# Optimization experiments

Hardware: AMD Instinct MI355X
Metric: run time of the kernel (lower is better)

Reference implementation:

```python
import jax, jax.numpy as jnp
import numpy as np

B, N, NKV = 2, 2048, 2048
E = 4096
H = 16
HD = E // H          # 256 head_dim
LQ = E // 8          # 512 q latent
LKV = E // 16        # 256 kv latent


def setup_inputs() -> dict:
    key = jax.random.key(0)
    ks = jax.random.split(key, 6)
    Q = jax.random.normal(ks[0], (B, N, E), dtype=jnp.float32)
    K = jax.random.normal(ks[1], (B, NKV, E), dtype=jnp.float32)
    # Linear weights stored as (in, out); scaled ~1/sqrt(fan_in) like torch default init
    Wq_d = jax.random.normal(ks[2], (E, LQ), dtype=jnp.float32) / np.sqrt(E)
    W_qk = jax.random.normal(ks[3], (LQ, H * LKV), dtype=jnp.float32) / np.sqrt(LQ)
    Wkv_d = jax.random.normal(ks[4], (E, LKV), dtype=jnp.float32) / np.sqrt(E)
    Wv_u = jax.random.normal(ks[5], (LKV, H * HD), dtype=jnp.float32) / np.sqrt(LKV)
    return {"Q": Q, "K": K, "Wq_d": Wq_d, "W_qk": W_qk, "Wkv_d": Wkv_d, "Wv_u": Wv_u}


def reference(Q, K, Wq_d, W_qk, Wkv_d, Wv_u):
    b, n, _ = Q.shape
    nkv = K.shape[1]
    C_q = Q @ Wq_d                                   # [B,N,Lq]
    C_kv = K @ Wkv_d                                 # [B,Nkv,Lkv]
    CqWqk = (C_q @ W_qk).reshape(b, n, H, LKV)       # [B,N,H,Lkv]
    # scores contract over the kv latent dim (absorbed-weight MLA)
    scores = jnp.einsum('bnhl,bkl->bhnk', CqWqk, C_kv) / jnp.sqrt(
        jnp.asarray(LKV, dtype=Q.dtype))             # [B,H,N,Nkv]
    attn = jax.nn.softmax(scores, axis=-1)
    V_up = (C_kv @ Wv_u).reshape(b, nkv, H, HD)      # [B,Nkv,H,hd]
    out = jnp.einsum('bhnk,bkhd->bnhd', attn, V_up)  # [B,N,H,hd]
    return out.reshape(b, n, H * HD)                 # [B,N,E]
```

## Files before the change

kernel.cpp:

```cpp
#include <hip/hip_runtime.h>


#define B_ 2
#define N_ 2048
#define H_ 16
#define HD_ 256
#define LKV_ 256

typedef __attribute__((ext_vector_type(8))) short bf8;
typedef __attribute__((ext_vector_type(4))) float f4;
typedef __attribute__((ext_vector_type(4))) unsigned short us4v;
typedef unsigned short u16;

__device__ __forceinline__ u16 f2b(float f) {
  union { float f; unsigned u; } v; v.f = f;
  unsigned r = (v.u + 0x7FFFu + ((v.u >> 16) & 1u)) >> 16;
  return (u16)r;
}

__device__ __forceinline__ void load_lds16(const void* g, void* l) {
  __builtin_amdgcn_global_load_lds(
      (const __attribute__((address_space(1))) unsigned int*)(unsigned long long)(uintptr_t)g,
      (__attribute__((address_space(3))) unsigned int*)(unsigned int)(uintptr_t)l,
      16, 0, 0);
}

__global__ __launch_bounds__(256) void cvt_bf16_2(const float* __restrict__ a,
                                                  u16* __restrict__ da,
                                                  const float* __restrict__ b,
                                                  u16* __restrict__ db, int n4)
{
  int i = blockIdx.x * 256 + threadIdx.x;
  const float* s; u16* d;
  if (i < n4) { s = a; d = da; } else { s = b; d = db; i -= n4; }
  float4 v = *(const float4*)(s + (size_t)i * 4);
  us4v o = {f2b(v.x), f2b(v.y), f2b(v.z), f2b(v.w)};
  *(us4v*)(d + (size_t)i * 4) = o;
}

__global__ __launch_bounds__(256) void cvt_transpose(const float* __restrict__ src,
                                                     u16* __restrict__ dst, int R, int C)
{
  __shared__ float tile[32][33];
  const int t = threadIdx.x;
  const int tr = t & 31, tc = t >> 5;
  const int r0 = blockIdx.x * 32, c0 = blockIdx.y * 32;
#pragma unroll
  for (int i = 0; i < 4; ++i)
    tile[tc + i * 8][tr] = src[(size_t)(r0 + tc + i * 8) * C + c0 + tr];
  __syncthreads();
#pragma unroll
  for (int i = 0; i < 4; ++i)
    dst[(size_t)(c0 + tc + i * 8) * R + r0 + tr] = f2b(tile[tr][tc + i * 8]);
}

__global__ __launch_bounds__(256) void gemm_bt(
    const u16* __restrict__ A,
    const u16* __restrict__ Bt,
    u16* __restrict__ C,
    int M, int N, int K)
{
  __shared__ u16 As[128 * 32];
  __shared__ u16 Bs[128 * 32];

  const int t = threadIdx.x;
  const int w = t >> 6, lane = t & 63;
  const int quad = lane >> 4, l16 = lane & 15;
  const int n0 = blockIdx.x * 128, m0 = blockIdx.y * 128;
  const int wm = (w >> 1) * 64, wn = (w & 1) * 64;

  f4 acc[4][4];
#pragma unroll
  for (int mi = 0; mi < 4; ++mi)
#pragma unroll
    for (int ni = 0; ni < 4; ++ni) acc[mi][ni] = (f4){0.f, 0.f, 0.f, 0.f};

  const u16* Ap = A + (size_t)m0 * K;
  const u16* Bp = Bt + (size_t)n0 * K;
  const int srow = t >> 2, spos = (t & 3) * 8;

  for (int k0 = 0; k0 < K; k0 += 32) {
    __syncthreads();
    load_lds16(Ap + (size_t)srow * K + k0 + spos,        &As[(size_t)t * 8]);
    load_lds16(Ap + (size_t)(srow + 64) * K + k0 + spos, &As[(size_t)(256 + t) * 8]);
    load_lds16(Bp + (size_t)srow * K + k0 + spos,        &Bs[(size_t)t * 8]);
    load_lds16(Bp + (size_t)(srow + 64) * K + k0 + spos, &Bs[(size_t)(256 + t) * 8]);
    __syncthreads();

    bf8 af[4], bfr[4];
#pragma unroll
    for (int mi = 0; mi < 4; ++mi)
      af[mi] = *(const bf8*)(&As[(wm + mi * 16 + l16) * 32 + quad * 8]);
#pragma unroll
    for (int ni = 0; ni < 4; ++ni)
      bfr[ni] = *(const bf8*)(&Bs[(wn + ni * 16 + l16) * 32 + quad * 8]);
#pragma unroll
    for (int mi = 0; mi < 4; ++mi)
#pragma unroll
      for (int ni = 0; ni < 4; ++ni)
        acc[mi][ni] = __builtin_amdgcn_mfma_f32_16x16x32_bf16(af[mi], bfr[ni], acc[mi][ni], 0, 0, 0);
  }

  u16* Cp = C + (size_t)m0 * N + n0;
#pragma unroll
  for (int mi = 0; mi < 4; ++mi)
#pragma unroll
    for (int r = 0; r < 4; ++r) {
      int m = wm + mi * 16 + quad * 4 + r;
#pragma unroll
      for (int ni = 0; ni < 4; ++ni)
        Cp[(size_t)m * N + wn + ni * 16 + l16] = f2b(acc[mi][ni][r]);
    }
}

__global__ __launch_bounds__(256) void gemm_qkv(
    const u16* __restrict__ Aq, const u16* __restrict__ Bq, u16* __restrict__ Cq,
    const u16* __restrict__ Ak, const u16* __restrict__ Bk, u16* __restrict__ Ck)
{
  const int K = 4096;
  __shared__ u16 As[128 * 32];
  __shared__ u16 Bs[64 * 32];

  const u16* A; const u16* Bt; u16* C; int N, n0;
  if (blockIdx.x < 8) { A = Aq; Bt = Bq; C = Cq; N = 512; n0 = blockIdx.x * 64; }
  else               { A = Ak; Bt = Bk; C = Ck; N = 256; n0 = (blockIdx.x - 8) * 64; }

  const int t = threadIdx.x;
  const int w = t >> 6, lane = t & 63;
  const int quad = lane >> 4, l16 = lane & 15;
  const int m0 = blockIdx.y * 128;
  const int wm = (w >> 1) * 64, wn = (w & 1) * 32;

  f4 acc[4][2];
#pragma unroll
  for (int mi = 0; mi < 4; ++mi)
#pragma unroll
    for (int ni = 0; ni < 2; ++ni) acc[mi][ni] = (f4){0.f, 0.f, 0.f, 0.f};

  const u16* Ap = A + (size_t)m0 * K;
  const u16* Bp = Bt + (size_t)n0 * K;
  const int srow = t >> 2, spos = (t & 3) * 8;

  for (int k0 = 0; k0 < K; k0 += 32) {
    __syncthreads();
    load_lds16(Ap + (size_t)srow * K + k0 + spos,        &As[(size_t)t * 8]);
    load_lds16(Ap + (size_t)(srow + 64) * K + k0 + spos, &As[(size_t)(256 + t) * 8]);
    load_lds16(Bp + (size_t)srow * K + k0 + spos,        &Bs[(size_t)t * 8]);
    __syncthreads();

    bf8 af[4], bfr[2];
#pragma unroll
    for (int mi = 0; mi < 4; ++mi)
      af[mi] = *(const bf8*)(&As[(wm + mi * 16 + l16) * 32 + quad * 8]);
#pragma unroll
    for (int ni = 0; ni < 2; ++ni)
      bfr[ni] = *(const bf8*)(&Bs[(wn + ni * 16 + l16) * 32 + quad * 8]);
#pragma unroll
    for (int mi = 0; mi < 4; ++mi)
#pragma unroll
      for (int ni = 0; ni < 2; ++ni)
        acc[mi][ni] = __builtin_amdgcn_mfma_f32_16x16x32_bf16(af[mi], bfr[ni], acc[mi][ni], 0, 0, 0);
  }

  u16* Cp = C + (size_t)m0 * N + n0;
#pragma unroll
  for (int mi = 0; mi < 4; ++mi)
#pragma unroll
    for (int r = 0; r < 4; ++r) {
      int m = wm + mi * 16 + quad * 4 + r;
#pragma unroll
      for (int ni = 0; ni < 2; ++ni)
        Cp[(size_t)m * N + wn + ni * 16 + l16] = f2b(acc[mi][ni][r]);
    }
}

__global__ __launch_bounds__(256) void transpose_v(const u16* __restrict__ vupB,
                                                   u16* __restrict__ vupT)
{
  __shared__ u16 tile[64][78];
  const int t = threadIdx.x;
  const int key0 = blockIdx.x * 64, d0 = blockIdx.y * 64;
  const int bh = blockIdx.z, b = bh >> 4, h = bh & 15;

#pragma unroll
  for (int i = 0; i < 2; ++i) {
    int c = t + 256 * i;
    int key = c >> 3, d8 = c & 7;
    bf8 v = *(const bf8*)(vupB + ((size_t)(b * N_ + key0 + key) * (H_ * HD_)) + h * HD_ + d0 + d8 * 8);
    *(bf8*)(&tile[key][d8 * 8]) = v;
  }
  __syncthreads();
#pragma unroll
  for (int i = 0; i < 2; ++i) {
    int c = t + 256 * i;
    int d = c >> 3, k8 = c & 7;
    bf8 v;
#pragma unroll
    for (int j = 0; j < 8; ++j) v[j] = (short)tile[k8 * 8 + j][d];
    *(bf8*)(vupT + ((size_t)bh * HD_ + d0 + d) * (size_t)N_ + key0 + k8 * 8) = v;
  }
}

__global__ __launch_bounds__(256, 3) void flash_mfma(
    const u16* __restrict__ q2b,
    const u16* __restrict__ ckvb,
    const u16* __restrict__ vupT,
    float* __restrict__ out)
{
  __shared__ u16 KtL[32 * 256];
  __shared__ u16 VtL[256 * 32];
  __shared__ u16 PtL[64 * 36];

  const int t = threadIdx.x;
  const int w = t >> 6, lane = t & 63;
  const int quad = lane >> 4, l16 = lane & 15;

  const int wg = blockIdx.x;
  const int xcd = wg & 7, idx = wg >> 3;
  const int bh = xcd * 4 + (idx >> 5);
  const int n0 = (idx & 31) * 64;
  const int b = bh >> 4, h = bh & 15;

  bf8 qf[8];
  {
    const u16* qbase = q2b + (size_t)(b * N_ + n0 + w * 16 + l16) * (H_ * LKV_) + h * LKV_ + quad * 8;
#pragma unroll
    for (int ks = 0; ks < 8; ++ks)
      qf[ks] = *(const bf8*)(qbase + ks * 32);
  }

  f4 o[16];
#pragma unroll
  for (int dt = 0; dt < 16; ++dt) o[dt] = (f4){0.f, 0.f, 0.f, 0.f};
  float ms[4], ls[4];
#pragma unroll
  for (int r = 0; r < 4; ++r) { ms[r] = -1e30f; ls[r] = 0.f; }

  const u16* kgb = ckvb + (size_t)b * N_ * LKV_;
  const u16* vgb = vupT + (size_t)bh * HD_ * N_;

  const int kswz = l16 & 7;
  const int vq8  = (quad ^ (l16 & 3)) * 8;

  for (int k0 = 0; k0 < N_; k0 += 32) {
    __syncthreads();
#pragma unroll
    for (int i = 0; i < 4; ++i) {
      int c = i * 256 + t;
      int kr = c >> 5, kc = (c & 31) ^ (kr & 7);
      load_lds16(kgb + (size_t)(k0 + kr) * LKV_ + kc * 8, &KtL[c * 8]);
    }
#pragma unroll
    for (int i = 0; i < 4; ++i) {
      int c = i * 256 + t;
      int vr = c >> 2, vc = (c & 3) ^ (vr & 3);
      load_lds16(vgb + (size_t)vr * N_ + k0 + vc * 8, &VtL[c * 8]);
    }
    __syncthreads();

    f4 sf[2];
    sf[0] = (f4){0,0,0,0}; sf[1] = (f4){0,0,0,0};
    __builtin_amdgcn_s_setprio(1);
#pragma unroll
    for (int nt = 0; nt < 2; ++nt) {
      const u16* kr = &KtL[(nt * 16 + l16) * 256];
#pragma unroll
      for (int ks = 0; ks < 8; ++ks) {
        bf8 kf = *(const bf8*)(kr + (((quad + ks * 4) ^ kswz) << 3));
        sf[nt] = __builtin_amdgcn_mfma_f32_16x16x32_bf16(qf[ks], kf, sf[nt], 0, 0, 0);
      }
    }
    __builtin_amdgcn_s_setprio(0);

    float al[4];
#pragma unroll
    for (int r = 0; r < 4; ++r) {
      float a0 = sf[0][r] * 0.0625f;
      float a1 = sf[1][r] * 0.0625f;
      float mx = fmaxf(a0, a1);
#pragma unroll
      for (int off = 1; off < 16; off <<= 1) mx = fmaxf(mx, __shfl_xor(mx, off, 16));
      float mn = fmaxf(ms[r], mx);
      float p0 = __expf(a0 - mn), p1 = __expf(a1 - mn);
      float sum = p0 + p1;
#pragma unroll
      for (int off = 1; off < 16; off <<= 1) sum += __shfl_xor(sum, off, 16);
      al[r] = __expf(ms[r] - mn);
      ls[r] = ls[r] * al[r] + sum;
      ms[r] = mn;
      int q = w * 16 + quad * 4 + r;
      PtL[q * 36 + l16]      = f2b(p0);
      PtL[q * 36 + 16 + l16] = f2b(p1);
    }
#pragma unroll
    for (int dt = 0; dt < 16; ++dt) {
      o[dt][0] *= al[0]; o[dt][1] *= al[1];
      o[dt][2] *= al[2]; o[dt][3] *= al[3];
    }

    bf8 pf = *(const bf8*)(&PtL[(w * 16 + l16) * 36 + quad * 8]);

    __builtin_amdgcn_s_setprio(1);
#pragma unroll
    for (int dt = 0; dt < 16; ++dt) {
      bf8 vf = *(const bf8*)(&VtL[(dt * 16 + l16) * 32 + vq8]);
      o[dt] = __builtin_amdgcn_mfma_f32_16x16x32_bf16(pf, vf, o[dt], 0, 0, 0);
    }
    __builtin_amdgcn_s_setprio(0);
  }

#pragma unroll
  for (int r = 0; r < 4; ++r) {
    float iv = 1.f / ls[r];
    float* dst = out + (size_t)(b * N_ + n0 + w * 16 + quad * 4 + r) * (H_ * HD_)
                 + h * HD_ + l16;
#pragma unroll
    for (int dt = 0; dt < 16; ++dt) dst[dt * 16] = o[dt][r] * iv;
  }
}

extern "C" void kernel_launch(void* const* d_in, const int* in_sizes, int n_in,
                              void* d_out, int out_size, void* d_ws, size_t ws_size,
                              hipStream_t stream) {
  const float* Q     = (const float*)d_in[0];
  const float* Kin   = (const float*)d_in[1];
  const float* Wq_d  = (const float*)d_in[2];
  const float* W_qk  = (const float*)d_in[3];
  const float* Wkv_d = (const float*)d_in[4];
  const float* Wv_u  = (const float*)d_in[5];
  float* out = (float*)d_out;

  char* ws = (char*)d_ws;
  u16* qbf   = (u16*)(ws);
  u16* vupT  = qbf;
  u16* kbf   = (u16*)(ws + 33554432);
  u16* vupB  = kbf;
  u16* q2b   = (u16*)(ws + 67108864);
  u16* cqb   = (u16*)(ws + 100663296);
  u16* ckvb  = (u16*)(ws + 104857600);
  u16* wqdT  = (u16*)(ws + 106954752);
  u16* wqkT  = (u16*)(ws + 111149056);
  u16* wkvdT = (u16*)(ws + 115343360);
  u16* wvuT  = (u16*)(ws + 117440512);

  cvt_bf16_2<<<dim3(32768), 256, 0, stream>>>(Q, qbf, Kin, kbf, 4194304);
  cvt_transpose<<<dim3(128, 16), 256, 0, stream>>>(Wq_d,  wqdT,  4096, 512);
  cvt_transpose<<<dim3(16, 128), 256, 0, stream>>>(W_qk,  wqkT,  512, 4096);
  cvt_transpose<<<dim3(128, 8),  256, 0, stream>>>(Wkv_d, wkvdT, 4096, 256);
  cvt_transpose<<<dim3(8, 128),  256, 0, stream>>>(Wv_u,  wvuT,  256, 4096);

  gemm_qkv<<<dim3(12, 32), 256, 0, stream>>>(qbf, wqdT, cqb, kbf, wkvdT, ckvb);
  gemm_bt<<<dim3(32, 32), 256, 0, stream>>>(cqb, wqkT, q2b, 4096, 4096, 512);
  gemm_bt<<<dim3(32, 32), 256, 0, stream>>>(ckvb, wvuT, vupB, 4096, 4096, 256);
  transpose_v<<<dim3(32, 4, 32), 256, 0, stream>>>(vupB, vupT);
  flash_mfma<<<dim3(1024), 256, 0, stream>>>(q2b, ckvb, vupT, out);
}
```

Baseline: 656.7 us.

## Give each flash-attention wave two query tiles and fold softmax scale into weights

The flash kernel now runs 2 waves of 128 threads per block, and each wave handles 32 query rows as two 16-row MFMA tiles. Every K and V fragment read from LDS is therefore reused for two MFMAs. The score MFMA operands are swapped so the row max and sum reductions take only two cross-quad shuffles. Row rescale factors and the final normalisers now pass through a small LDS array. The 1/16 softmax scale is folded into the bf16 conversion of W_qk, which removes the per-element multiply. In exchange, register pressure roughly doubles (o[2][16], qf[2][8]), each thread issues twice as many async loads, and per-block parallelism is halved.

```diff
diff --git a/kernel.cpp b/kernel.cpp
--- a/kernel.cpp
+++ b/kernel.cpp
@@ -39,7 +39,8 @@
 }
 
 __global__ __launch_bounds__(256) void cvt_transpose(const float* __restrict__ src,
-                                                     u16* __restrict__ dst, int R, int C)
+                                                     u16* __restrict__ dst, int R, int C,
+                                                     float scale)
 {
   __shared__ float tile[32][33];
   const int t = threadIdx.x;
@@ -51,7 +52,7 @@
   __syncthreads();
 #pragma unroll
   for (int i = 0; i < 4; ++i)
-    dst[(size_t)(c0 + tc + i * 8) * R + r0 + tr] = f2b(tile[tr][tc + i * 8]);
+    dst[(size_t)(c0 + tc + i * 8) * R + r0 + tr] = f2b(tile[tr][tc + i * 8] * scale);
 }
 
 __global__ __launch_bounds__(256) void gemm_bt(
@@ -201,7 +202,7 @@
   }
 }
 
-__global__ __launch_bounds__(256, 3) void flash_mfma(
+__global__ __launch_bounds__(128, 2) void flash_mfma(
     const u16* __restrict__ q2b,
     const u16* __restrict__ ckvb,
     const u16* __restrict__ vupT,
@@ -209,7 +210,8 @@
 {
   __shared__ u16 KtL[32 * 256];
   __shared__ u16 VtL[256 * 32];
-  __shared__ u16 PtL[64 * 36];
+  __shared__ u16 PtL[64 * 40];
+  __shared__ float alL[64];
 
   const int t = threadIdx.x;
   const int w = t >> 6, lane = t & 63;
@@ -221,45 +223,48 @@
   const int n0 = (idx & 31) * 64;
   const int b = bh >> 4, h = bh & 15;
 
-  bf8 qf[8];
+  bf8 qf[2][8];
   {
-    const u16* qbase = q2b + (size_t)(b * N_ + n0 + w * 16 + l16) * (H_ * LKV_) + h * LKV_ + quad * 8;
-#pragma unroll
-    for (int ks = 0; ks < 8; ++ks)
-      qf[ks] = *(const bf8*)(qbase + ks * 32);
-  }
-
-  f4 o[16];
-#pragma unroll
-  for (int dt = 0; dt < 16; ++dt) o[dt] = (f4){0.f, 0.f, 0.f, 0.f};
-  float ms[4], ls[4];
-#pragma unroll
-  for (int r = 0; r < 4; ++r) { ms[r] = -1e30f; ls[r] = 0.f; }
+    const u16* qbase = q2b + (size_t)(b * N_ + n0 + w * 32 + l16) * (H_ * LKV_) + h * LKV_ + quad * 8;
+#pragma unroll
+    for (int mi = 0; mi < 2; ++mi)
+#pragma unroll
+      for (int ks = 0; ks < 8; ++ks)
+        qf[mi][ks] = *(const bf8*)(qbase + (size_t)(mi * 16) * (H_ * LKV_) + ks * 32);
+  }
+
+  f4 o[2][16];
+#pragma unroll
+  for (int mi = 0; mi < 2; ++mi)
+#pragma unroll
+    for (int dt = 0; dt < 16; ++dt) o[mi][dt] = (f4){0.f, 0.f, 0.f, 0.f};
+  float ms[2] = {-1e30f, -1e30f}, ls[2] = {0.f, 0.f};
 
   const u16* kgb = ckvb + (size_t)b * N_ * LKV_;
   const u16* vgb = vupT + (size_t)bh * HD_ * N_;
 
   const int kswz = l16 & 7;
-  const int vq8  = (quad ^ (l16 & 3)) * 8;
+  const int vsl8 = (quad ^ ((l16 >> 1) & 3)) * 8;
 
   for (int k0 = 0; k0 < N_; k0 += 32) {
     __syncthreads();
 #pragma unroll
-    for (int i = 0; i < 4; ++i) {
-      int c = i * 256 + t;
+    for (int i = 0; i < 8; ++i) {
+      int c = i * 128 + t;
       int kr = c >> 5, kc = (c & 31) ^ (kr & 7);
       load_lds16(kgb + (size_t)(k0 + kr) * LKV_ + kc * 8, &KtL[c * 8]);
     }
 #pragma unroll
-    for (int i = 0; i < 4; ++i) {
-      int c = i * 256 + t;
-      int vr = c >> 2, vc = (c & 3) ^ (vr & 3);
+    for (int i = 0; i < 8; ++i) {
+      int c = i * 128 + t;
+      int vr = c >> 2, vc = (c & 3) ^ ((vr >> 1) & 3);
       load_lds16(vgb + (size_t)vr * N_ + k0 + vc * 8, &VtL[c * 8]);
     }
     __syncthreads();
 
-    f4 sf[2];
-    sf[0] = (f4){0,0,0,0}; sf[1] = (f4){0,0,0,0};
+    f4 sf[2][2];
+    sf[0][0] = (f4){0,0,0,0}; sf[0][1] = (f4){0,0,0,0};
+    sf[1][0] = (f4){0,0,0,0}; sf[1][1] = (f4){0,0,0,0};
     __builtin_amdgcn_s_setprio(1);
 #pragma unroll
     for (int nt = 0; nt < 2; ++nt) {
@@ -267,56 +272,82 @@
 #pragma unroll
       for (int ks = 0; ks < 8; ++ks) {
         bf8 kf = *(const bf8*)(kr + (((quad + ks * 4) ^ kswz) << 3));
-        sf[nt] = __builtin_amdgcn_mfma_f32_16x16x32_bf16(qf[ks], kf, sf[nt], 0, 0, 0);
+        sf[0][nt] = __builtin_amdgcn_mfma_f32_16x16x32_bf16(kf, qf[0][ks], sf[0][nt], 0, 0, 0);
+        sf[1][nt] = __builtin_amdgcn_mfma_f32_16x16x32_bf16(kf, qf[1][ks], sf[1][nt], 0, 0, 0);
       }
     }
     __builtin_amdgcn_s_setprio(0);
 
-    float al[4];
+#pragma unroll
+    for (int mi = 0; mi < 2; ++mi) {
+      float mx = sf[mi][0][0];
+#pragma unroll
+      for (int r = 1; r < 4; ++r) mx = fmaxf(mx, sf[mi][0][r]);
+#pragma unroll
+      for (int r = 0; r < 4; ++r) mx = fmaxf(mx, sf[mi][1][r]);
+      mx = fmaxf(mx, __shfl_xor(mx, 16));
+      mx = fmaxf(mx, __shfl_xor(mx, 32));
+      float mn = fmaxf(ms[mi], mx);
+      float p0[4], p1[4];
+      float sum = 0.f;
+#pragma unroll
+      for (int r = 0; r < 4; ++r) { p0[r] = __expf(sf[mi][0][r] - mn); sum += p0[r]; }
+#pragma unroll
+      for (int r = 0; r < 4; ++r) { p1[r] = __expf(sf[mi][1][r] - mn); sum += p1[r]; }
+      sum += __shfl_xor(sum, 16);
+      sum += __shfl_xor(sum, 32);
+      float al = __expf(ms[mi] - mn);
+      ls[mi] = ls[mi] * al + sum;
+      ms[mi] = mn;
+      int q = w * 32 + mi * 16 + l16;
+      us4v pk0 = {f2b(p0[0]), f2b(p0[1]), f2b(p0[2]), f2b(p0[3])};
+      us4v pk1 = {f2b(p1[0]), f2b(p1[1]), f2b(p1[2]), f2b(p1[3])};
+      *(us4v*)(&PtL[q * 40 + quad * 4])      = pk0;
+      *(us4v*)(&PtL[q * 40 + 16 + quad * 4]) = pk1;
+      if (quad == 0) alL[q] = al;
+    }
+
+#pragma unroll
+    for (int mi = 0; mi < 2; ++mi) {
+      float a0 = alL[w * 32 + mi * 16 + quad * 4 + 0];
+      float a1 = alL[w * 32 + mi * 16 + quad * 4 + 1];
+      float a2 = alL[w * 32 + mi * 16 + quad * 4 + 2];
+      float a3 = alL[w * 32 + mi * 16 + quad * 4 + 3];
+#pragma unroll
+      for (int dt = 0; dt < 16; ++dt) {
+        o[mi][dt][0] *= a0; o[mi][dt][1] *= a1;
+        o[mi][dt][2] *= a2; o[mi][dt][3] *= a3;
+      }
+    }
+
+    bf8 pf0 = *(const bf8*)(&PtL[(w * 32 + l16) * 40 + quad * 8]);
+    bf8 pf1 = *(const bf8*)(&PtL[(w * 32 + 16 + l16) * 40 + quad * 8]);
+
+    __builtin_amdgcn_s_setprio(1);
+#pragma unroll
+    for (int dt = 0; dt < 16; ++dt) {
+      bf8 vf = *(const bf8*)(&VtL[(dt * 16 + l16) * 32 + vsl8]);
+      o[0][dt] = __builtin_amdgcn_mfma_f32_16x16x32_bf16(pf0, vf, o[0][dt], 0, 0, 0);
+      o[1][dt] = __builtin_amdgcn_mfma_f32_16x16x32_bf16(pf1, vf, o[1][dt], 0, 0, 0);
+    }
+    __builtin_amdgcn_s_setprio(0);
+  }
+
+  if (quad == 0) {
+    alL[w * 32 + l16]      = ls[0];
+    alL[w * 32 + 16 + l16] = ls[1];
+  }
+  __syncthreads();
+#pragma unroll
+  for (int mi = 0; mi < 2; ++mi)
 #pragma unroll
     for (int r = 0; r < 4; ++r) {
-      float a0 = sf[0][r] * 0.0625f;
-      float a1 = sf[1][r] * 0.0625f;
-      float mx = fmaxf(a0, a1);
-#pragma unroll
-      for (int off = 1; off < 16; off <<= 1) mx = fmaxf(mx, __shfl_xor(mx, off, 16));
-      float mn = fmaxf(ms[r], mx);
-      float p0 = __expf(a0 - mn), p1 = __expf(a1 - mn);
-      float sum = p0 + p1;
-#pragma unroll
-      for (int off = 1; off < 16; off <<= 1) sum += __shfl_xor(sum, off, 16);
-      al[r] = __expf(ms[r] - mn);
-      ls[r] = ls[r] * al[r] + sum;
-      ms[r] = mn;
-      int q = w * 16 + quad * 4 + r;
-      PtL[q * 36 + l16]      = f2b(p0);
-      PtL[q * 36 + 16 + l16] = f2b(p1);
-    }
-#pragma unroll
-    for (int dt = 0; dt < 16; ++dt) {
-      o[dt][0] *= al[0]; o[dt][1] *= al[1];
-      o[dt][2] *= al[2]; o[dt][3] *= al[3];
-    }
-
-    bf8 pf = *(const bf8*)(&PtL[(w * 16 + l16) * 36 + quad * 8]);
-
-    __builtin_amdgcn_s_setprio(1);
-#pragma unroll
-    for (int dt = 0; dt < 16; ++dt) {
-      bf8 vf = *(const bf8*)(&VtL[(dt * 16 + l16) * 32 + vq8]);
-      o[dt] = __builtin_amdgcn_mfma_f32_16x16x32_bf16(pf, vf, o[dt], 0, 0, 0);
-    }
-    __builtin_amdgcn_s_setprio(0);
-  }
-
-#pragma unroll
-  for (int r = 0; r < 4; ++r) {
-    float iv = 1.f / ls[r];
-    float* dst = out + (size_t)(b * N_ + n0 + w * 16 + quad * 4 + r) * (H_ * HD_)
-                 + h * HD_ + l16;
-#pragma unroll
-    for (int dt = 0; dt < 16; ++dt) dst[dt * 16] = o[dt][r] * iv;
-  }
+      float iv = 1.f / alL[w * 32 + mi * 16 + quad * 4 + r];
+      float* dst = out + (size_t)(b * N_ + n0 + w * 32 + mi * 16 + quad * 4 + r) * (H_ * HD_)
+                   + h * HD_ + l16;
+#pragma unroll
+      for (int dt = 0; dt < 16; ++dt) dst[dt * 16] = o[mi][dt][r] * iv;
+    }
 }
 
 extern "C" void kernel_launch(void* const* d_in, const int* in_sizes, int n_in,
@@ -344,14 +375,14 @@
   u16* wvuT  = (u16*)(ws + 117440512);
 
   cvt_bf16_2<<<dim3(32768), 256, 0, stream>>>(Q, qbf, Kin, kbf, 4194304);
-  cvt_transpose<<<dim3(128, 16), 256, 0, stream>>>(Wq_d,  wqdT,  4096, 512);
-  cvt_transpose<<<dim3(16, 128), 256, 0, stream>>>(W_qk,  wqkT,  512, 4096);
-  cvt_transpose<<<dim3(128, 8),  256, 0, stream>>>(Wkv_d, wkvdT, 4096, 256);
-  cvt_transpose<<<dim3(8, 128),  256, 0, stream>>>(Wv_u,  wvuT,  256, 4096);
+  cvt_transpose<<<dim3(128, 16), 256, 0, stream>>>(Wq_d,  wqdT,  4096, 512, 1.f);
+  cvt_transpose<<<dim3(16, 128), 256, 0, stream>>>(W_qk,  wqkT,  512, 4096, 0.0625f);
+  cvt_transpose<<<dim3(128, 8),  256, 0, stream>>>(Wkv_d, wkvdT, 4096, 256, 1.f);
+  cvt_transpose<<<dim3(8, 128),  256, 0, stream>>>(Wv_u,  wvuT,  256, 4096, 1.f);
 
   gemm_qkv<<<dim3(12, 32), 256, 0, stream>>>(qbf, wqdT, cqb, kbf, wkvdT, ckvb);
   gemm_bt<<<dim3(32, 32), 256, 0, stream>>>(cqb, wqkT, q2b, 4096, 4096, 512);
   gemm_bt<<<dim3(32, 32), 256, 0, stream>>>(ckvb, wvuT, vupB, 4096, 4096, 256);
   transpose_v<<<dim3(32, 4, 32), 256, 0, stream>>>(vupB, vupT);
-  flash_mfma<<<dim3(1024), 256, 0, stream>>>(q2b, ckvb, vupT, out);
-}
+  flash_mfma<<<dim3(1024), 128, 0, stream>>>(q2b, ckvb, vupT, out);
+}
```

Result: no change. 664.5 us (+1.2%).
